# Optimization experiments

Measured on AMD Instinct MI355X. Metric: run time of the kernel, lower is better.

## Reference

```python
import jax, jax.numpy as jnp
import numpy as np

B, T, D, K, CAND = 1024, 256, 128, 4, 500
NEG = float(-2**32 + 1)
EPS = 1e-3  # keras LayerNormalization default epsilon

def ln(x, g, b):
    mu = jnp.mean(x, axis=-1, keepdims=True)
    var = jnp.mean(jnp.square(x - mu), axis=-1, keepdims=True)
    return (x - mu) * jax.lax.rsqrt(var + EPS) * g + b

def setup_inputs() -> dict:
    key = jax.random.key(0)
    ks = jax.random.split(key, 12)
    s = 0.05
    inp = {
        'item_his_eb': jax.random.normal(ks[0], (B, T, D), jnp.float32),
        'mask': jax.random.randint(ks[1], (B, T), 0, 2, jnp.int32),
        'W1': jax.random.normal(ks[2], (D, D), jnp.float32) * s,
        'W2': jax.random.normal(ks[3], (D,), jnp.float32) * s,
        'W3': jax.random.normal(ks[4], (D, D), jnp.float32) * s,
        'W4': jax.random.normal(ks[5], (D,), jnp.float32) * s,
        'W_k1': jax.random.normal(ks[6], (K, D, D), jnp.float32) * s,
        'W_k2': jax.random.normal(ks[7], (K, D), jnp.float32) * s,
        'C': jax.random.normal(ks[8], (CAND, D), jnp.float32) * s,
        'pos_emb': jax.random.normal(ks[9], (1, T, D), jnp.float32) * s,
        'g1': jnp.ones((D,), jnp.float32), 'b1': jnp.zeros((D,), jnp.float32),
        'g2': jnp.ones((D,), jnp.float32), 'b2': jnp.zeros((D,), jnp.float32),
        'g3': jnp.ones((D,), jnp.float32), 'b3': jnp.zeros((D,), jnp.float32),
        'g4': jnp.ones((D,), jnp.float32), 'b4': jnp.zeros((D,), jnp.float32),
    }
    return inp

def reference(item_his_eb, mask, W1, W2, W3, W4, W_k1, W_k2, C, pos_emb,
              g1, b1, g2, b2, g3, b3, g4, b4):
    num_interest = W_k1.shape[0]
    m0 = (mask == 0)  # [B,T] padding positions
    x = item_his_eb + pos_emb  # [B,T,D]

    # Concept activation
    hidden = jnp.tanh(jnp.einsum('bte,ea->bta', x, W1))
    att = jnp.einsum('bte,e->bt', hidden, W2)
    a = jax.nn.softmax(jnp.where(m0, NEG, att), axis=-1)
    z_u = jnp.einsum('bte,bt->be', x, a)
    s_u = jnp.einsum('be,ce->bc', z_u, C)  # [B,CAND]
    s_u_k, idx = jax.lax.top_k(s_u, num_interest)  # sorted descending
    c_u = C[idx] * jax.nn.sigmoid(s_u_k)[..., None]  # [B,K,D]

    # Interest embedding generation
    h1 = jnp.einsum('bte,ea->bta', x, W3)
    h1 = jnp.einsum('bte,bke->btk', ln(h1, g1, b1), ln(c_u, g2, b2))
    h1 = jnp.where(m0[:, :, None], NEG, h1)
    P_kt = jnp.transpose(jax.nn.softmax(h1, axis=-1), (0, 2, 1))  # [B,K,T]
    h2 = jnp.tanh(jnp.einsum('bte,kea->bkta', x, W_k1))
    h2 = jnp.einsum('bkte,ke->bkt', h2, W_k2)
    h2 = jnp.where(m0[:, None, :], NEG, h2)
    P_tk = jax.nn.softmax(h2, axis=-1)  # softmax over t
    P = P_kt * P_tk
    interest_emb = ln(jnp.einsum('bte,bkt->bke', x, P), g3, b3)  # [B,K,D]

    # Interest aggregation
    P_u = jnp.transpose(P_kt, (0, 2, 1))  # [B,T,K]
    X_hat = jnp.einsum('btk,bke->bte', P_u, c_u)
    h3 = jnp.tanh(jnp.einsum('bte,ea->bta', X_hat, W3))
    h3 = jnp.einsum('bte,e->bt', h3, W4)
    h3 = jax.nn.softmax(jnp.where(m0, NEG, h3), axis=-1)
    c_apt = ln(jnp.einsum('bte,bt->be', X_hat, h3), g4, b4)
    e_u = jax.nn.softmax(jnp.einsum('be,bke->bk', c_apt, interest_emb) / 0.1, axis=-1)
    v_u = jnp.einsum('bke,bk->be', interest_emb, e_u)
    return v_u
```

## Files before the change

kernel.cpp:

```cpp
#include <hip/hip_runtime.h>
#include <hip/hip_bf16.h>
#include <string.h>

#define BB 1024
#define TT 256
#define DD 128
#define KK 4
#define CC 500
#define BR 64
#define NEGF (-4294967296.0f)
#define EPSL 1e-3f

typedef __attribute__((ext_vector_type(8))) short bf16x8;
typedef __attribute__((ext_vector_type(4))) float f32x4;


__device__ __forceinline__ float fast_tanh(float x){
  float ax = fabsf(x);
  float e  = __expf(2.0f * ax);
  float t  = 1.0f - 2.0f * __builtin_amdgcn_rcpf(e + 1.0f);
  return copysignf(t, x);
}

__device__ __forceinline__ unsigned short bfbits(float f){
  __hip_bfloat16 h = __float2bfloat16(f);
  unsigned short u;
  memcpy(&u, &h, 2);
  return u;
}
__device__ __forceinline__ float bf2f(unsigned short u){
  return __uint_as_float(((unsigned)u) << 16);
}

__device__ __forceinline__ float wave_sum(float v){
  #pragma unroll
  for (int o = 32; o > 0; o >>= 1) v += __shfl_xor(v, o);
  return v;
}
__device__ __forceinline__ float wave_max(float v){
  #pragma unroll
  for (int o = 32; o > 0; o >>= 1) v = fmaxf(v, __shfl_xor(v, o));
  return v;
}


__global__ __launch_bounds__(256) void k_preppack(
    const float* __restrict__ W1, const float* __restrict__ W3,
    const float* __restrict__ Wk1, const float* __restrict__ Cmat,
    uint4* __restrict__ whi, uint4* __restrict__ wlo,
    float* __restrict__ W3T, float* __restrict__ CT)
{
  int gid = blockIdx.x * 256 + threadIdx.x;
  if (gid < 12288){
    int lane = gid & 63;
    int frag = gid >> 6;
    int n = frag & 7, kt = (frag >> 3) & 3, w = frag >> 5;
    const float* Wp = (w == 0) ? W1 : (w == 1) ? W3 : (Wk1 + (long)(w - 2) * DD * DD);
    int col = n * 16 + (lane & 15);
    int k0 = kt * 32 + (lane >> 4) * 8;
    unsigned int H[4], L[4];
    #pragma unroll
    for (int d = 0; d < 4; ++d){
      float v0 = Wp[(long)(k0 + 2 * d) * DD + col];
      float v1 = Wp[(long)(k0 + 2 * d + 1) * DD + col];
      unsigned short h0 = bfbits(v0); unsigned short l0 = bfbits(v0 - bf2f(h0));
      unsigned short h1 = bfbits(v1); unsigned short l1 = bfbits(v1 - bf2f(h1));
      H[d] = (unsigned)h0 | ((unsigned)h1 << 16);
      L[d] = (unsigned)l0 | ((unsigned)l1 << 16);
    }
    whi[gid] = make_uint4(H[0], H[1], H[2], H[3]);
    wlo[gid] = make_uint4(L[0], L[1], L[2], L[3]);
  } else {
    int j = gid - 12288;
    if (j < DD * DD){
      int a = j >> 7, e = j & 127;
      W3T[j] = W3[e * DD + a];
    } else {
      j -= DD * DD;
      if (j < DD * CC){
        int e = j / CC, c = j - e * CC;
        CT[j] = Cmat[c * DD + e];
      }
    }
  }
}


__global__ __launch_bounds__(512, 8) void k_big6m(
    const float* __restrict__ item, const float* __restrict__ pos,
    const uint4* __restrict__ whi, const uint4* __restrict__ wlo,
    const float* __restrict__ W2, const float* __restrict__ Wk2,
    float* __restrict__ att, float* __restrict__ h2log, float* __restrict__ lnstats)
{
  __shared__ uint4 smem4[2048];
  __shared__ float dscr[5][BR][2];
  __shared__ float sscr[2][BR][2];
  char* smem = (char*)smem4;
  const int tid = threadIdx.x, lane = tid & 63, wv = tid >> 6;
  const int ni = wv & 1, mi = wv >> 1;
  const long rbase = (long)blockIdx.x * BR;
  const int r15 = lane & 15, g = lane >> 4;
  const f32x4 ZV = {0.f, 0.f, 0.f, 0.f};

  #pragma unroll
  for (int it = 0; it < 2; ++it){
    int cid = tid + it * 512;
    int row = cid >> 4, c0 = (cid & 15) * 8;
    const float* src = item + (rbase + row) * DD + c0;
    const float* ps  = pos + (int)((rbase + row) & 255) * DD + c0;
    float4 f0 = *(const float4*)src;
    float4 f1 = *(const float4*)(src + 4);
    float4 p0 = *(const float4*)ps;
    float4 p1 = *(const float4*)(ps + 4);
    float v[8] = {f0.x + p0.x, f0.y + p0.y, f0.z + p0.z, f0.w + p0.w,
                  f1.x + p1.x, f1.y + p1.y, f1.z + p1.z, f1.w + p1.w};
    unsigned int H[4], L[4];
    #pragma unroll
    for (int d = 0; d < 4; ++d){
      unsigned short h0 = bfbits(v[2 * d]);     unsigned short l0 = bfbits(v[2 * d]     - bf2f(h0));
      unsigned short h1 = bfbits(v[2 * d + 1]); unsigned short l1 = bfbits(v[2 * d + 1] - bf2f(h1));
      H[d] = (unsigned)h0 | ((unsigned)h1 << 16);
      L[d] = (unsigned)l0 | ((unsigned)l1 << 16);
    }
    int byt = (c0 * 2) ^ ((row & 7) << 4);
    *(uint4*)(smem + row * 256 + byt)         = make_uint4(H[0], H[1], H[2], H[3]);
    *(uint4*)(smem + 16384 + row * 256 + byt) = make_uint4(L[0], L[1], L[2], L[3]);
  }
  __syncthreads();

  const int wrow = mi * 16;
  const int WL6[6] = {0, 2, 3, 4, 5, 1};

  #pragma unroll
  for (int wi = 0; wi < 6; ++wi){
    const int w = WL6[wi];
    f32x4 acc[4];
    #pragma unroll
    for (int n = 0; n < 4; ++n) acc[n] = ZV;

    #pragma unroll
    for (int kt = 0; kt < 4; ++kt){
      int row = wrow + r15;
      int byt = (kt * 64 + g * 16) ^ ((row & 7) << 4);
      bf16x8 ah = *(const bf16x8*)(smem + row * 256 + byt);
      bf16x8 al = *(const bf16x8*)(smem + 16384 + row * 256 + byt);
      const uint4* bhp = whi + (long)((w * 4 + kt) * 8 + ni * 4) * 64 + lane;
      const uint4* blp = wlo + (long)((w * 4 + kt) * 8 + ni * 4) * 64 + lane;
      #pragma unroll
      for (int n = 0; n < 4; ++n){
        uint4 bhu = bhp[n * 64], blu = blp[n * 64];
        bf16x8 bh = *(const bf16x8*)&bhu;
        bf16x8 bl = *(const bf16x8*)&blu;
        acc[n] = __builtin_amdgcn_mfma_f32_16x16x32_bf16(ah, bh, acc[n], 0, 0, 0);
        acc[n] = __builtin_amdgcn_mfma_f32_16x16x32_bf16(ah, bl, acc[n], 0, 0, 0);
        acc[n] = __builtin_amdgcn_mfma_f32_16x16x32_bf16(al, bh, acc[n], 0, 0, 0);
      }
    }

    if (w != 1){
      const float* vp = (w == 0) ? W2 : (Wk2 + (w - 2) * DD);
      float pd[4] = {0.f, 0.f, 0.f, 0.f};
      #pragma unroll
      for (int n = 0; n < 4; ++n){
        float vv = vp[ni * 64 + n * 16 + r15];
        #pragma unroll
        for (int j = 0; j < 4; ++j)
          pd[j] = fmaf(fast_tanh(acc[n][j]), vv, pd[j]);
      }
      #pragma unroll
      for (int j = 0; j < 4; ++j){
        float v = pd[j];
        v += __shfl_xor(v, 1); v += __shfl_xor(v, 2);
        v += __shfl_xor(v, 4); v += __shfl_xor(v, 8);
        if (r15 == 0) dscr[wi][wrow + g * 4 + j][ni] = v;
      }
    } else {
      #pragma unroll
      for (int j = 0; j < 4; ++j){
        float s = 0.f, q = 0.f;
        #pragma unroll
        for (int n = 0; n < 4; ++n){
          float y = acc[n][j];
          s += y; q = fmaf(y, y, q);
        }
        s += __shfl_xor(s, 1); s += __shfl_xor(s, 2);
        s += __shfl_xor(s, 4); s += __shfl_xor(s, 8);
        q += __shfl_xor(q, 1); q += __shfl_xor(q, 2);
        q += __shfl_xor(q, 4); q += __shfl_xor(q, 8);
        if (r15 == 0){
          int row = wrow + g * 4 + j;
          sscr[0][row][ni] = s;
          sscr[1][row][ni] = q;
        }
      }
    }
  }
  __syncthreads();

  if (tid < BR){
    long rg = rbase + tid;
    long b = rg >> 8; int t = (int)(rg & 255);
    att[rg] = dscr[0][tid][0] + dscr[0][tid][1];
    #pragma unroll
    for (int wi = 1; wi < 5; ++wi)
      h2log[(b * KK + (wi - 1)) * TT + t] = dscr[wi][tid][0] + dscr[wi][tid][1];
    float s = sscr[0][tid][0] + sscr[0][tid][1];
    float q = sscr[1][tid][0] + sscr[1][tid][1];
    float mu = s * (1.f / DD);
    float var = q * (1.f / DD) - mu * mu;
    float rs = rsqrtf(var + EPSL);
    float2 st; st.x = mu; st.y = rs;
    *(float2*)&lnstats[rg * 2] = st;
  }
}


__global__ __launch_bounds__(256, 4) void k_fused(
    const float* __restrict__ item, const float* __restrict__ pos,
    const int* __restrict__ mask, const float* __restrict__ att,
    const float* __restrict__ h2log, const float* __restrict__ lnstats,
    const float* __restrict__ Cmat, const float* __restrict__ CT,
    const float* __restrict__ W3, const float* __restrict__ W3T,
    const float* __restrict__ g1, const float* __restrict__ b1,
    const float* __restrict__ g2, const float* __restrict__ b2,
    const float* __restrict__ g3, const float* __restrict__ b3,
    const float* __restrict__ g4, const float* __restrict__ b4,
    const float* __restrict__ W4, float* __restrict__ out)
{
  __shared__ float arena[4096];
  __shared__ float pkt_s[KK][TT];
  __shared__ float P_s[KK][TT];
  __shared__ float lnc_s[KK][DD];
  __shared__ float cu_s[KK][DD];
  __shared__ float vk_s[KK][DD];
  __shared__ float cw3s[KK][DD];
  __shared__ float ies_s[KK][DD];
  __shared__ float a_s[TT];
  __shared__ int   m0s[TT];
  __shared__ float g1s[DD], b1s[DD];
  __shared__ float cas[DD], w4s[DD];
  __shared__ float rbuf[32];
  __shared__ float sel_v[KK];
  __shared__ int   sel_i[KK];
  __shared__ float SkTk[2][KK];

  const int tid = threadIdx.x;
  const long b = blockIdx.x;
  const int lane = tid & 63, wv = tid >> 6;

  float attv = att[b * TT + tid];
  int   mk   = mask[b * TT + tid];
  if (tid < DD){ g1s[tid] = g1[tid]; b1s[tid] = b1[tid]; }
  m0s[tid] = (mk == 0);

  {
    float v = (mk == 0) ? NEGF : attv;
    float wm = wave_max(v);
    if (lane == 0) rbuf[wv] = wm;
    __syncthreads();
    float mx = fmaxf(fmaxf(rbuf[0], rbuf[1]), fmaxf(rbuf[2], rbuf[3]));
    float ex = __expf(v - mx);
    float ws = wave_sum(ex);
    if (lane == 0) rbuf[4 + wv] = ws;
    __syncthreads();
    float sm = rbuf[4] + rbuf[5] + rbuf[6] + rbuf[7];
    a_s[tid] = ex / sm;
  }
  __syncthreads();

  const float4* item4 = (const float4*)(item + (long)b * TT * DD);
  const float4* pos4  = (const float4*)pos;

  {
    int q = tid & 31, h = tid >> 5;
    float4 acc = {0.f, 0.f, 0.f, 0.f};
    for (int t = h; t < TT; t += 8){
      float4 xi = item4[t * 32 + q];
      float4 pp = pos4[t * 32 + q];
      float av = a_s[t];
      acc.x = fmaf(av, xi.x + pp.x, acc.x);
      acc.y = fmaf(av, xi.y + pp.y, acc.y);
      acc.z = fmaf(av, xi.z + pp.z, acc.z);
      acc.w = fmaf(av, xi.w + pp.w, acc.w);
    }
    *(float4*)&arena[h * 128 + q * 4] = acc;
    __syncthreads();
    if (tid < DD){
      float z = 0.f;
      #pragma unroll
      for (int h2 = 0; h2 < 8; ++h2) z += arena[h2 * 128 + tid];
      arena[1024 + tid] = z;
    }
    __syncthreads();
  }
  float* zs  = arena + 1024;
  float* s_s = arena + 1152;

  for (int c = tid; c < 512; c += 256){
    float s = -3.0e38f;
    if (c < CC){
      s = 0.f;
      for (int e = 0; e < DD; ++e) s = fmaf(zs[e], CT[e * CC + c], s);
    }
    s_s[c] = s;
  }
  __syncthreads();

  for (int k = 0; k < KK; ++k){
    float bv = -3.0e38f; int bi = 1 << 20;
    for (int c = tid; c < 512; c += 256){
      float sv = s_s[c];
      if (sv > bv || (sv == bv && c < bi)){ bv = sv; bi = c; }
    }
    #pragma unroll
    for (int o = 32; o > 0; o >>= 1){
      float ov = __shfl_xor(bv, o); int oi = __shfl_xor(bi, o);
      if (ov > bv || (ov == bv && oi < bi)){ bv = ov; bi = oi; }
    }
    if (lane == 0){ rbuf[wv] = bv; ((int*)rbuf)[8 + wv] = bi; }
    __syncthreads();
    if (tid == 0){
      float xv = rbuf[0]; int xi = ((int*)rbuf)[8];
      #pragma unroll
      for (int w2 = 1; w2 < 4; ++w2){
        float ov = rbuf[w2]; int oi = ((int*)rbuf)[8 + w2];
        if (ov > xv || (ov == xv && oi < xi)){ xv = ov; xi = oi; }
      }
      sel_v[k] = xv; sel_i[k] = xi; s_s[xi] = -3.0e38f;
    }
    __syncthreads();
  }

  {
    int k = wv, e0 = lane, e1 = lane + 64;
    float sig = 1.f / (1.f + __expf(-sel_v[k]));
    long ci = (long)sel_i[k] * DD;
    float c0 = Cmat[ci + e0] * sig, c1 = Cmat[ci + e1] * sig;
    cu_s[k][e0] = c0; cu_s[k][e1] = c1;
    float mean = wave_sum(c0 + c1) * (1.f / DD);
    float d0 = c0 - mean, d1 = c1 - mean;
    float var = wave_sum(d0 * d0 + d1 * d1) * (1.f / DD);
    float rs = rsqrtf(var + EPSL);
    float l0 = d0 * rs * g2[e0] + b2[e0];
    float l1 = d1 * rs * g2[e1] + b2[e1];
    lnc_s[k][e0] = l0; lnc_s[k][e1] = l1;
    float gl0 = g1s[e0] * l0, gl1 = g1s[e1] * l1;
    float S = wave_sum(gl0 + gl1);
    float T = wave_sum(b1s[e0] * l0 + b1s[e1] * l1);
    if (lane == 0){ SkTk[0][k] = S; SkTk[1][k] = T; }
    cw3s[k][e0] = gl0; cw3s[k][e1] = gl1;
    float v0 = 0.f, v1 = 0.f;
    for (int a = 0; a < DD; ++a){
      float gv = cw3s[k][a];
      v0 = fmaf(W3T[a * DD + e0], gv, v0);
      v1 = fmaf(W3T[a * DD + e1], gv, v1);
    }
    vk_s[k][e0] = v0; vk_s[k][e1] = v1;
  }
  __syncthreads();

  for (int step = 0; step < 16; ++step){
    int t = step * 16 + wv * 4 + (lane >> 4);
    int e0 = (lane & 15) * 8;
    const float* xr = item + ((long)b * TT + t) * DD + e0;
    const float* pr = pos + t * DD + e0;
    float4 xa = *(const float4*)xr, xb = *(const float4*)(xr + 4);
    float4 pa = *(const float4*)pr, pb = *(const float4*)(pr + 4);
    float x0 = xa.x + pa.x, x1 = xa.y + pa.y, x2 = xa.z + pa.z, x3 = xa.w + pa.w;
    float x4 = xb.x + pb.x, x5 = xb.y + pb.y, x6 = xb.z + pb.z, x7 = xb.w + pb.w;
    float2 st = *(const float2*)&lnstats[((long)b * TT + t) * 2];
    float h[KK];
    #pragma unroll
    for (int k = 0; k < KK; ++k){
      float4 v0 = *(const float4*)&vk_s[k][e0];
      float4 v1 = *(const float4*)&vk_s[k][e0 + 4];
      float pk = x0 * v0.x + x1 * v0.y + x2 * v0.z + x3 * v0.w
               + x4 * v1.x + x5 * v1.y + x6 * v1.z + x7 * v1.w;
      pk += __shfl_xor(pk, 1); pk += __shfl_xor(pk, 2);
      pk += __shfl_xor(pk, 4); pk += __shfl_xor(pk, 8);
      h[k] = st.y * (pk - st.x * SkTk[0][k]) + SkTk[1][k];
    }
    float p[KK];
    if (m0s[t]){
      p[0] = p[1] = p[2] = p[3] = 0.25f;
    } else {
      float mxh = fmaxf(fmaxf(h[0], h[1]), fmaxf(h[2], h[3]));
      float sme = 0.f;
      #pragma unroll
      for (int k = 0; k < KK; ++k){ p[k] = __expf(h[k] - mxh); sme += p[k]; }
      float inv = 1.f / sme;
      #pragma unroll
      for (int k = 0; k < KK; ++k) p[k] *= inv;
    }
    int kk = lane & 15;
    if (kk < KK) pkt_s[kk][t] = p[kk];
  }
  __syncthreads();

  {
    int k = wv;
    float4 vj = *(const float4*)&h2log[((long)b * KK + k) * TT + lane * 4];
    float v0 = m0s[lane * 4 + 0] ? NEGF : vj.x;
    float v1 = m0s[lane * 4 + 1] ? NEGF : vj.y;
    float v2 = m0s[lane * 4 + 2] ? NEGF : vj.z;
    float v3 = m0s[lane * 4 + 3] ? NEGF : vj.w;
    float mxv = wave_max(fmaxf(fmaxf(v0, v1), fmaxf(v2, v3)));
    float e0 = __expf(v0 - mxv), e1 = __expf(v1 - mxv);
    float e2 = __expf(v2 - mxv), e3 = __expf(v3 - mxv);
    float sm = wave_sum(e0 + e1 + e2 + e3);
    float inv = 1.f / sm;
    float4 pk4 = *(const float4*)&pkt_s[k][lane * 4];
    float4 r;
    r.x = pk4.x * e0 * inv; r.y = pk4.y * e1 * inv;
    r.z = pk4.z * e2 * inv; r.w = pk4.w * e3 * inv;
    *(float4*)&P_s[k][lane * 4] = r;
  }
  __syncthreads();

  {
    int q = tid & 31, h = tid >> 5;
    float4 ak[KK];
    #pragma unroll
    for (int k = 0; k < KK; ++k) ak[k] = {0.f, 0.f, 0.f, 0.f};
    for (int t = h; t < TT; t += 8){
      float4 xi = item4[t * 32 + q];
      float4 pp = pos4[t * 32 + q];
      float4 xv; xv.x = xi.x + pp.x; xv.y = xi.y + pp.y; xv.z = xi.z + pp.z; xv.w = xi.w + pp.w;
      #pragma unroll
      for (int k = 0; k < KK; ++k){
        float pv = P_s[k][t];
        ak[k].x = fmaf(pv, xv.x, ak[k].x); ak[k].y = fmaf(pv, xv.y, ak[k].y);
        ak[k].z = fmaf(pv, xv.z, ak[k].z); ak[k].w = fmaf(pv, xv.w, ak[k].w);
      }
    }
    #pragma unroll
    for (int k = 0; k < KK; ++k)
      *(float4*)&arena[h * 512 + k * 128 + q * 4] = ak[k];
    __syncthreads();
    int e = tid & 127, kh = tid >> 7;
    for (int k2 = kh; k2 < KK; k2 += 2){
      float s = 0.f;
      #pragma unroll
      for (int h2 = 0; h2 < 8; ++h2) s += arena[h2 * 512 + k2 * 128 + e];
      ies_s[k2][e] = s;
    }
  }
  __syncthreads();

  {
    int k = wv, e0 = lane, e1 = lane + 64;
    float v0 = ies_s[k][e0], v1 = ies_s[k][e1];
    float mean = wave_sum(v0 + v1) * (1.f / DD);
    float d0 = v0 - mean, d1 = v1 - mean;
    float var = wave_sum(d0 * d0 + d1 * d1) * (1.f / DD);
    float rs = rsqrtf(var + EPSL);
    ies_s[k][e0] = d0 * rs * g3[e0] + b3[e0];
    ies_s[k][e1] = d1 * rs * g3[e1] + b3[e1];
    float s0 = 0.f, s1 = 0.f;
    for (int e = 0; e < DD; ++e){
      float cv = cu_s[k][e];
      s0 = fmaf(cv, W3[e * DD + e0], s0);
      s1 = fmaf(cv, W3[e * DD + e1], s1);
    }
    cw3s[k][e0] = s0; cw3s[k][e1] = s1;
  }
  if (tid < DD) w4s[tid] = W4[tid];
  __syncthreads();

  float pk0 = pkt_s[0][tid], pk1 = pkt_s[1][tid], pk2 = pkt_s[2][tid], pk3 = pkt_s[3][tid];
  float sv = 0.f;
  for (int a = 0; a < DD; ++a){
    float hp = pk0 * cw3s[0][a] + pk1 * cw3s[1][a] + pk2 * cw3s[2][a] + pk3 * cw3s[3][a];
    sv = fmaf(fast_tanh(hp), w4s[a], sv);
  }
  float h3;
  {
    float v = m0s[tid] ? NEGF : sv;
    float wm = wave_max(v);
    if (lane == 0) rbuf[wv] = wm;
    __syncthreads();
    float mx = fmaxf(fmaxf(rbuf[0], rbuf[1]), fmaxf(rbuf[2], rbuf[3]));
    float ex = __expf(v - mx);
    float ws = wave_sum(ex);
    if (lane == 0) rbuf[4 + wv] = ws;
    __syncthreads();
    float sm = rbuf[4] + rbuf[5] + rbuf[6] + rbuf[7];
    h3 = ex / sm;
  }
  __syncthreads();
  {
    float w0 = wave_sum(pk0 * h3), w1 = wave_sum(pk1 * h3);
    float w2 = wave_sum(pk2 * h3), w3 = wave_sum(pk3 * h3);
    if (lane == 0){
      rbuf[8 + wv * 4 + 0] = w0; rbuf[8 + wv * 4 + 1] = w1;
      rbuf[8 + wv * 4 + 2] = w2; rbuf[8 + wv * 4 + 3] = w3;
    }
  }
  __syncthreads();
  float wk0 = rbuf[8] + rbuf[12] + rbuf[16] + rbuf[20];
  float wk1 = rbuf[9] + rbuf[13] + rbuf[17] + rbuf[21];
  float wk2 = rbuf[10] + rbuf[14] + rbuf[18] + rbuf[22];
  float wk3 = rbuf[11] + rbuf[15] + rbuf[19] + rbuf[23];
  {
    float cp = 0.f;
    if (tid < DD)
      cp = wk0 * cu_s[0][tid] + wk1 * cu_s[1][tid] + wk2 * cu_s[2][tid] + wk3 * cu_s[3][tid];
    float ws = wave_sum((tid < DD) ? cp : 0.f);
    if (lane == 0) rbuf[wv] = ws;
    __syncthreads();
    float mean = (rbuf[0] + rbuf[1] + rbuf[2] + rbuf[3]) * (1.f / DD);
    float d = (tid < DD) ? cp - mean : 0.f;
    float wq = wave_sum(d * d);
    if (lane == 0) rbuf[4 + wv] = wq;
    __syncthreads();
    float var = (rbuf[4] + rbuf[5] + rbuf[6] + rbuf[7]) * (1.f / DD);
    float rs = rsqrtf(var + EPSL);
    if (tid < DD) cas[tid] = d * rs * g4[tid] + b4[tid];
  }
  __syncthreads();
  {
    float c0 = (tid < DD) ? cas[tid] * ies_s[0][tid] : 0.f;
    float c1 = (tid < DD) ? cas[tid] * ies_s[1][tid] : 0.f;
    float c2 = (tid < DD) ? cas[tid] * ies_s[2][tid] : 0.f;
    float c3 = (tid < DD) ? cas[tid] * ies_s[3][tid] : 0.f;
    float w0 = wave_sum(c0), w1 = wave_sum(c1), w2 = wave_sum(c2), w3 = wave_sum(c3);
    if (lane == 0){
      rbuf[8 + wv * 4 + 0] = w0; rbuf[8 + wv * 4 + 1] = w1;
      rbuf[8 + wv * 4 + 2] = w2; rbuf[8 + wv * 4 + 3] = w3;
    }
    __syncthreads();
    float l0 = (rbuf[8] + rbuf[12] + rbuf[16] + rbuf[20]) * 10.f;
    float l1 = (rbuf[9] + rbuf[13] + rbuf[17] + rbuf[21]) * 10.f;
    float l2 = (rbuf[10] + rbuf[14] + rbuf[18] + rbuf[22]) * 10.f;
    float l3 = (rbuf[11] + rbuf[15] + rbuf[19] + rbuf[23]) * 10.f;
    float mx2 = fmaxf(fmaxf(l0, l1), fmaxf(l2, l3));
    float e0 = __expf(l0 - mx2), e1 = __expf(l1 - mx2);
    float e2 = __expf(l2 - mx2), e3 = __expf(l3 - mx2);
    float inv = 1.f / (e0 + e1 + e2 + e3);
    if (tid < DD){
      float r = (ies_s[0][tid] * e0 + ies_s[1][tid] * e1 +
                 ies_s[2][tid] * e2 + ies_s[3][tid] * e3) * inv;
      out[b * DD + tid] = r;
    }
  }
}


extern "C" void kernel_launch(void* const* d_in, const int* in_sizes, int n_in,
                              void* d_out, int out_size, void* d_ws, size_t ws_size,
                              hipStream_t stream)
{
  const float* item = (const float*)d_in[0];
  const int*   mask = (const int*)d_in[1];
  const float* W1   = (const float*)d_in[2];
  const float* W2   = (const float*)d_in[3];
  const float* W3   = (const float*)d_in[4];
  const float* W4   = (const float*)d_in[5];
  const float* Wk1  = (const float*)d_in[6];
  const float* Wk2  = (const float*)d_in[7];
  const float* Cm   = (const float*)d_in[8];
  const float* pos  = (const float*)d_in[9];
  const float* g1   = (const float*)d_in[10]; const float* b1 = (const float*)d_in[11];
  const float* g2   = (const float*)d_in[12]; const float* b2 = (const float*)d_in[13];
  const float* g3   = (const float*)d_in[14]; const float* b3 = (const float*)d_in[15];
  const float* g4   = (const float*)d_in[16]; const float* b4 = (const float*)d_in[17];
  float* out = (float*)d_out;

  char* p = (char*)d_ws;
  float* att     = (float*)(p);
  float* h2log   = (float*)(p + 1048576);
  float* lnstats = (float*)(p + 5242880);
  float* W3T     = (float*)(p + 7340032);
  float* CT      = (float*)(p + 7405568);
  uint4* whi = (uint4*)d_out;
  uint4* wlo = whi + 12288;
  (void)in_sizes; (void)n_in; (void)out_size; (void)ws_size;

  k_preppack <<<dim3(362), dim3(256), 0, stream>>>(W1, W3, Wk1, Cm, whi, wlo, W3T, CT);
  k_big6m    <<<dim3((BB * TT) / BR), dim3(512), 0, stream>>>(item, pos, whi, wlo, W2, Wk2,
                                                              att, h2log, lnstats);
  k_fused    <<<dim3(BB), dim3(256), 0, stream>>>(item, pos, mask, att, h2log, lnstats,
                                                  Cm, CT, W3, W3T,
                                                  g1, b1, g2, b2, g3, b3, g4, b4, W4, out);
}
```

Baseline: 347.2 us.

## Retile big GEMM kernel: 128 rows per block, weights as A operand

```diff
diff --git a/kernel.cpp b/kernel.cpp
--- a/kernel.cpp
+++ b/kernel.cpp
@@ -7,7 +7,6 @@
 #define DD 128
 #define KK 4
 #define CC 500
-#define BR 64
 #define NEGF (-4294967296.0f)
 #define EPSL 1e-3f
 
@@ -86,24 +85,25 @@
 }
 
 
-__global__ __launch_bounds__(512, 8) void k_big6m(
+__global__ __launch_bounds__(512, 4) void k_big6m(
     const float* __restrict__ item, const float* __restrict__ pos,
     const uint4* __restrict__ whi, const uint4* __restrict__ wlo,
     const float* __restrict__ W2, const float* __restrict__ Wk2,
     float* __restrict__ att, float* __restrict__ h2log, float* __restrict__ lnstats)
 {
-  __shared__ uint4 smem4[2048];
-  __shared__ float dscr[5][BR][2];
-  __shared__ float sscr[2][BR][2];
+  __shared__ uint4 smem4[4096];
+  __shared__ float vsh[5][DD];
+  __shared__ float dscr[5][128];
+  __shared__ float sscr[2][128];
   char* smem = (char*)smem4;
   const int tid = threadIdx.x, lane = tid & 63, wv = tid >> 6;
-  const int ni = wv & 1, mi = wv >> 1;
-  const long rbase = (long)blockIdx.x * BR;
+  const int tt = wv;
+  const long rbase = (long)blockIdx.x * 128;
   const int r15 = lane & 15, g = lane >> 4;
   const f32x4 ZV = {0.f, 0.f, 0.f, 0.f};
 
   #pragma unroll
-  for (int it = 0; it < 2; ++it){
+  for (int it = 0; it < 4; ++it){
     int cid = tid + it * 512;
     int row = cid >> 4, c0 = (cid & 15) * 8;
     const float* src = item + (rbase + row) * DD + c0;
@@ -124,88 +124,82 @@
     }
     int byt = (c0 * 2) ^ ((row & 7) << 4);
     *(uint4*)(smem + row * 256 + byt)         = make_uint4(H[0], H[1], H[2], H[3]);
-    *(uint4*)(smem + 16384 + row * 256 + byt) = make_uint4(L[0], L[1], L[2], L[3]);
-  }
-  __syncthreads();
-
-  const int wrow = mi * 16;
+    *(uint4*)(smem + 32768 + row * 256 + byt) = make_uint4(L[0], L[1], L[2], L[3]);
+  }
+  for (int i = tid; i < 5 * DD; i += 512){
+    int w = i >> 7, f = i & 127;
+    vsh[w][f] = (w == 0) ? W2[f] : Wk2[(w - 1) * DD + f];
+  }
+  __syncthreads();
+
   const int WL6[6] = {0, 2, 3, 4, 5, 1};
 
   #pragma unroll
   for (int wi = 0; wi < 6; ++wi){
     const int w = WL6[wi];
-    f32x4 acc[4];
-    #pragma unroll
-    for (int n = 0; n < 4; ++n) acc[n] = ZV;
-
+    f32x4 acc[8];
+    #pragma unroll
+    for (int nf = 0; nf < 8; ++nf) acc[nf] = ZV;
+
+    __builtin_amdgcn_s_setprio(1);
     #pragma unroll
     for (int kt = 0; kt < 4; ++kt){
-      int row = wrow + r15;
+      int row = tt * 16 + r15;
       int byt = (kt * 64 + g * 16) ^ ((row & 7) << 4);
-      bf16x8 ah = *(const bf16x8*)(smem + row * 256 + byt);
-      bf16x8 al = *(const bf16x8*)(smem + 16384 + row * 256 + byt);
-      const uint4* bhp = whi + (long)((w * 4 + kt) * 8 + ni * 4) * 64 + lane;
-      const uint4* blp = wlo + (long)((w * 4 + kt) * 8 + ni * 4) * 64 + lane;
-      #pragma unroll
-      for (int n = 0; n < 4; ++n){
-        uint4 bhu = bhp[n * 64], blu = blp[n * 64];
-        bf16x8 bh = *(const bf16x8*)&bhu;
-        bf16x8 bl = *(const bf16x8*)&blu;
-        acc[n] = __builtin_amdgcn_mfma_f32_16x16x32_bf16(ah, bh, acc[n], 0, 0, 0);
-        acc[n] = __builtin_amdgcn_mfma_f32_16x16x32_bf16(ah, bl, acc[n], 0, 0, 0);
-        acc[n] = __builtin_amdgcn_mfma_f32_16x16x32_bf16(al, bh, acc[n], 0, 0, 0);
+      bf16x8 bh = *(const bf16x8*)(smem + row * 256 + byt);
+      bf16x8 bl = *(const bf16x8*)(smem + 32768 + row * 256 + byt);
+      const uint4* ahp = whi + (long)((w * 4 + kt) * 8) * 64 + lane;
+      const uint4* alp = wlo + (long)((w * 4 + kt) * 8) * 64 + lane;
+      #pragma unroll
+      for (int nf = 0; nf < 8; ++nf){
+        uint4 ahu = ahp[nf * 64], alu = alp[nf * 64];
+        bf16x8 ah = *(const bf16x8*)&ahu;
+        bf16x8 al = *(const bf16x8*)&alu;
+        acc[nf] = __builtin_amdgcn_mfma_f32_16x16x32_bf16(ah, bh, acc[nf], 0, 0, 0);
+        acc[nf] = __builtin_amdgcn_mfma_f32_16x16x32_bf16(ah, bl, acc[nf], 0, 0, 0);
+        acc[nf] = __builtin_amdgcn_mfma_f32_16x16x32_bf16(al, bh, acc[nf], 0, 0, 0);
       }
     }
+    __builtin_amdgcn_s_setprio(0);
 
     if (w != 1){
-      const float* vp = (w == 0) ? W2 : (Wk2 + (w - 2) * DD);
-      float pd[4] = {0.f, 0.f, 0.f, 0.f};
-      #pragma unroll
-      for (int n = 0; n < 4; ++n){
-        float vv = vp[ni * 64 + n * 16 + r15];
+      float pd = 0.f;
+      #pragma unroll
+      for (int nf = 0; nf < 8; ++nf)
         #pragma unroll
         for (int j = 0; j < 4; ++j)
-          pd[j] = fmaf(fast_tanh(acc[n][j]), vv, pd[j]);
-      }
-      #pragma unroll
-      for (int j = 0; j < 4; ++j){
-        float v = pd[j];
-        v += __shfl_xor(v, 1); v += __shfl_xor(v, 2);
-        v += __shfl_xor(v, 4); v += __shfl_xor(v, 8);
-        if (r15 == 0) dscr[wi][wrow + g * 4 + j][ni] = v;
-      }
+          pd = fmaf(fast_tanh(acc[nf][j]), vsh[wi][nf * 16 + g * 4 + j], pd);
+      pd += __shfl_xor(pd, 16);
+      pd += __shfl_xor(pd, 32);
+      if (lane < 16) dscr[wi][tt * 16 + lane] = pd;
     } else {
-      #pragma unroll
-      for (int j = 0; j < 4; ++j){
-        float s = 0.f, q = 0.f;
+      float s = 0.f, q = 0.f;
+      #pragma unroll
+      for (int nf = 0; nf < 8; ++nf)
         #pragma unroll
-        for (int n = 0; n < 4; ++n){
-          float y = acc[n][j];
+        for (int j = 0; j < 4; ++j){
+          float y = acc[nf][j];
           s += y; q = fmaf(y, y, q);
         }
-        s += __shfl_xor(s, 1); s += __shfl_xor(s, 2);
-        s += __shfl_xor(s, 4); s += __shfl_xor(s, 8);
-        q += __shfl_xor(q, 1); q += __shfl_xor(q, 2);
-        q += __shfl_xor(q, 4); q += __shfl_xor(q, 8);
-        if (r15 == 0){
-          int row = wrow + g * 4 + j;
-          sscr[0][row][ni] = s;
-          sscr[1][row][ni] = q;
-        }
+      s += __shfl_xor(s, 16); s += __shfl_xor(s, 32);
+      q += __shfl_xor(q, 16); q += __shfl_xor(q, 32);
+      if (lane < 16){
+        sscr[0][tt * 16 + lane] = s;
+        sscr[1][tt * 16 + lane] = q;
       }
     }
   }
   __syncthreads();
 
-  if (tid < BR){
+  if (tid < 128){
     long rg = rbase + tid;
     long b = rg >> 8; int t = (int)(rg & 255);
-    att[rg] = dscr[0][tid][0] + dscr[0][tid][1];
+    att[rg] = dscr[0][tid];
     #pragma unroll
     for (int wi = 1; wi < 5; ++wi)
-      h2log[(b * KK + (wi - 1)) * TT + t] = dscr[wi][tid][0] + dscr[wi][tid][1];
-    float s = sscr[0][tid][0] + sscr[0][tid][1];
-    float q = sscr[1][tid][0] + sscr[1][tid][1];
+      h2log[(b * KK + (wi - 1)) * TT + t] = dscr[wi][tid];
+    float s = sscr[0][tid];
+    float q = sscr[1][tid];
     float mu = s * (1.f / DD);
     float var = q * (1.f / DD) - mu * mu;
     float rs = rsqrtf(var + EPSL);
@@ -577,8 +571,8 @@
   (void)in_sizes; (void)n_in; (void)out_size; (void)ws_size;
 
   k_preppack <<<dim3(362), dim3(256), 0, stream>>>(W1, W3, Wk1, Cm, whi, wlo, W3T, CT);
-  k_big6m    <<<dim3((BB * TT) / BR), dim3(512), 0, stream>>>(item, pos, whi, wlo, W2, Wk2,
-                                                              att, h2log, lnstats);
+  k_big6m    <<<dim3((BB * TT) / 128), dim3(512), 0, stream>>>(item, pos, whi, wlo, W2, Wk2,
+                                                               att, h2log, lnstats);
   k_fused    <<<dim3(BB), dim3(256), 0, stream>>>(item, pos, mask, att, h2log, lnstats,
                                                   Cm, CT, W3, W3T,
                                                   g1, b1, g2, b2, g3, b3, g4, b4, W4, out);
```

Measured after the change: 337.9 us. 2.7% less time.
